# Kernel optimization log

Measured on AMD Instinct MI355X. Metric: run time of the kernel, lower is better.

Reference implementation:

```python
import jax, jax.numpy as jnp
import numpy as np

ROPE_THETA = 10000.0


def _rope(t, offset):
    """lucidrains-style interleaved RoPE. t: [b, s, h, d]."""
    s, d = t.shape[1], t.shape[-1]
    inv_freq = 1.0 / (ROPE_THETA ** (jnp.arange(0, d, 2, dtype=jnp.float32) / d))
    pos = jnp.arange(s, dtype=jnp.float32) + offset
    freqs = pos[:, None] * inv_freq[None, :]            # [s, d/2]
    freqs = jnp.repeat(freqs, 2, axis=-1)               # [s, d] interleaved
    cos = jnp.cos(freqs)[None, :, None, :].astype(t.dtype)
    sin = jnp.sin(freqs)[None, :, None, :].astype(t.dtype)
    x1 = t[..., 0::2]
    x2 = t[..., 1::2]
    rot = jnp.stack((-x2, x1), axis=-1).reshape(t.shape)  # rotate_half, interleaved
    return t * cos + rot * sin


def setup_inputs() -> dict:
    key = jax.random.key(0)
    ks = jax.random.split(key, 7)
    B, T, P, D, H, Hd = 4, 1024, 1024, 2048, 16, 128
    sc = 0.02
    return {
        "x": jax.random.normal(ks[0], (B, T, D), jnp.float32),
        "past_k": jax.random.normal(ks[1], (B, P, H, Hd), jnp.float32),
        "past_v": jax.random.normal(ks[2], (B, P, H, Hd), jnp.float32),
        "Wq": jax.random.normal(ks[3], (D, D), jnp.float32) * sc,
        "Wk": jax.random.normal(ks[4], (D, D), jnp.float32) * sc,
        "Wv": jax.random.normal(ks[5], (D, D), jnp.float32) * sc,
        "Wo": jax.random.normal(ks[6], (D, D), jnp.float32) * sc,
    }


def reference(x, past_k, past_v, Wq, Wk, Wv, Wo):
    B, T, D = x.shape
    H = past_k.shape[2]
    Hd = D // H
    P = past_k.shape[1]

    # QKV projections (bias-free) + head split: 'b t (h f) -> b t h f'
    q = (x @ Wq).reshape(B, T, H, Hd)
    k_new = (x @ Wk).reshape(B, T, H, Hd)
    v_new = (x @ Wv).reshape(B, T, H, Hd)

    # KV-cache concat along seq dim (-3)
    k = jnp.concatenate((past_k, k_new), axis=1)  # [B, P+T, H, Hd]
    v = jnp.concatenate((past_v, v_new), axis=1)

    # RoPE: K over full past+new from position 0; Q with offset = past length
    k = _rope(k, 0)
    q = _rope(q, P)

    # Flash-attn causal semantics (bottom-right aligned): q_i sees kv_j, j <= i + P
    scale = 1.0 / np.sqrt(Hd)
    scores = jnp.einsum("bthd,bshd->bhts", q, k) * scale  # [B, H, T, P+T]
    iq = jnp.arange(T)[:, None]
    jk = jnp.arange(P + T)[None, :]
    mask = jk <= (iq + P)
    scores = jnp.where(mask[None, None], scores, jnp.finfo(scores.dtype).min)
    attn = jax.nn.softmax(scores, axis=-1)
    y = jnp.einsum("bhts,bshd->bthd", attn, v)            # [B, T, H, Hd]

    y = y.reshape(B, T, D) @ Wo                            # output proj
    return y
```

## Files before the change

kernel.cpp:

```cpp
#include <hip/hip_runtime.h>

typedef unsigned short u16;
typedef float f32x4 __attribute__((ext_vector_type(4)));
typedef short bf16x8 __attribute__((ext_vector_type(8)));

#define GLOAD16(gp, lp) __builtin_amdgcn_global_load_lds( \
    (const __attribute__((address_space(1))) void*)(gp),  \
    (__attribute__((address_space(3))) void*)(lp), 16, 0, 0)

__device__ __forceinline__ float bf2f(u16 u) {
  union { unsigned int i; float f; } v; v.i = ((unsigned int)u) << 16; return v.f;
}
__device__ __forceinline__ u16 f2bf(float f) {
  unsigned int u = __float_as_uint(f);
  u += 0x7FFFu + ((u >> 16) & 1u);
  return (u16)(u >> 16);
}

__global__ void trig_kernel(float2* __restrict__ trig) {
  int idx = blockIdx.x * 256 + threadIdx.x;
  int pos = idx >> 6, i = idx & 63;
  double invf = pow(10000.0, -(double)i / 64.0);
  float ang = (float)pos * (float)invf;
  trig[idx] = make_float2(cosf(ang), sinf(ang));
}

__global__ void convert_x(const float* __restrict__ src, u16* __restrict__ dst) {
  size_t idx = (size_t)blockIdx.x * 256 + threadIdx.x;
  float4 v = *(const float4*)&src[idx * 4];
  *(ushort4*)&dst[idx * 4] = make_ushort4(f2bf(v.x), f2bf(v.y), f2bf(v.z), f2bf(v.w));
}

__global__ void transpose_w(const float* __restrict__ src, u16* __restrict__ dst) {
  __shared__ u16 tile[128][129];
  int k0 = blockIdx.x * 128, n0 = blockIdx.y * 128;
  int t = threadIdx.x;
  for (int j = 0; j < 16; ++j) {
    int flat = j * 1024 + t * 4;
    int r = flat >> 7, cl = flat & 127;
    float4 v = *(const float4*)&src[(size_t)(k0 + r) * 2048 + n0 + cl];
    tile[r][cl] = f2bf(v.x); tile[r][cl+1] = f2bf(v.y);
    tile[r][cl+2] = f2bf(v.z); tile[r][cl+3] = f2bf(v.w);
  }
  __syncthreads();
  for (int j = 0; j < 16; ++j) {
    int flat = j * 1024 + t * 4;
    int r = flat >> 7, cl = flat & 127;
    ushort4 o = make_ushort4(tile[cl][r], tile[cl+1][r], tile[cl+2][r], tile[cl+3][r]);
    *(ushort4*)&dst[(size_t)(n0 + r) * 2048 + k0 + cl] = o;
  }
}

template<int WF32>
__global__ void __launch_bounds__(256) gemm_bt(
    const u16* __restrict__ A, const u16* __restrict__ Bt,
    void* __restrict__ Cp, int ldc, int nbx, int kt_iters, int lda, int ldb)
{
  __shared__ __align__(16) u16 lds_a[4096];
  __shared__ __align__(16) u16 lds_b[4096];
  int nb = gridDim.x;
  int per = nb >> 3;
  int bid = blockIdx.x;
  int sw = (bid & 7) * per + (bid >> 3);
  int bm = sw / nbx, bn = sw % nbx;
  int tid = threadIdx.x, w = tid >> 6, lane = tid & 63;
  int wy = w >> 1, wx = w & 1, g = lane >> 4, c16 = lane & 15;

  const u16* ga0 = A  + (size_t)(bm * 128 + (2*w+0) * 16 + c16) * lda + g * 8;
  const u16* ga1 = A  + (size_t)(bm * 128 + (2*w+1) * 16 + c16) * lda + g * 8;
  const u16* gb0 = Bt + (size_t)(bn * 128 + (2*w+0) * 16 + c16) * ldb + g * 8;
  const u16* gb1 = Bt + (size_t)(bn * 128 + (2*w+1) * 16 + c16) * ldb + g * 8;
  u16* la0 = &lds_a[(2*w+0) * 512]; u16* la1 = &lds_a[(2*w+1) * 512];
  u16* lb0 = &lds_b[(2*w+0) * 512]; u16* lb1 = &lds_b[(2*w+1) * 512];

  f32x4 acc[4][4];
  const f32x4 vzero = {0.f, 0.f, 0.f, 0.f};
  #pragma unroll
  for (int i = 0; i < 4; ++i)
    #pragma unroll
    for (int j = 0; j < 4; ++j) acc[i][j] = vzero;

  for (int kt = 0; kt < kt_iters; ++kt) {
    int ko = kt * 32;
    __syncthreads();
    GLOAD16(ga0 + ko, la0); GLOAD16(ga1 + ko, la1);
    GLOAD16(gb0 + ko, lb0); GLOAD16(gb1 + ko, lb1);
    __syncthreads();
    bf16x8 af[4], bfv[4];
    #pragma unroll
    for (int f = 0; f < 4; ++f) af[f]  = *(const bf16x8*)&lds_a[(wy*4 + f) * 512 + lane * 8];
    #pragma unroll
    for (int f = 0; f < 4; ++f) bfv[f] = *(const bf16x8*)&lds_b[(wx*4 + f) * 512 + lane * 8];
    #pragma unroll
    for (int i = 0; i < 4; ++i)
      #pragma unroll
      for (int j = 0; j < 4; ++j)
        acc[i][j] = __builtin_amdgcn_mfma_f32_16x16x32_bf16(af[i], bfv[j], acc[i][j], 0, 0, 0);
  }

  #pragma unroll
  for (int i = 0; i < 4; ++i)
    #pragma unroll
    for (int j = 0; j < 4; ++j)
      #pragma unroll
      for (int r = 0; r < 4; ++r) {
        size_t row = (size_t)bm * 128 + wy * 64 + i * 16 + 4 * g + r;
        size_t col = (size_t)bn * 128 + wx * 64 + j * 16 + c16;
        if (WF32) ((float*)Cp)[row * ldc + col] = acc[i][j][r];
        else      ((u16*)Cp)[row * ldc + col]   = f2bf(acc[i][j][r]);
      }
}

__global__ void rope_q(u16* __restrict__ C1, const float2* __restrict__ trig) {
  int idx = blockIdx.x * 256 + threadIdx.x;
  int row = idx >> 10;
  int pi = idx & 1023;
  int h = pi >> 6, i = pi & 63;
  int pos = 1024 + (row & 1023);
  float2 cs = trig[pos * 64 + i];
  u16* p = &C1[(size_t)row * 6144 + h * 128 + 2 * i];
  ushort2 xv = *(const ushort2*)p;
  float x0 = bf2f(xv.x), x1 = bf2f(xv.y);
  const float SC = 0.088388347648318447f * 1.4426950408889634f;
  float y0 = (x0 * cs.x - x1 * cs.y) * SC;
  float y1 = (x1 * cs.x + x0 * cs.y) * SC;
  *(ushort2*)p = make_ushort2(f2bf(y0), f2bf(y1));
}

__global__ void build_k(const float* __restrict__ past_k, const u16* __restrict__ C1,
                        const float2* __restrict__ trig, u16* __restrict__ Kb) {
  int idx = blockIdx.x * 256 + threadIdx.x;
  int i = idx & 63;
  int s = (idx >> 6) & 2047;
  int bh = idx >> 17;
  int b = bh >> 4, h = bh & 15;
  float x0, x1;
  if (s < 1024) {
    const float* p = &past_k[(size_t)((b * 1024 + s) * 16 + h) * 128 + 2 * i];
    float2 v = *(const float2*)p;
    x0 = v.x; x1 = v.y;
  } else {
    ushort2 v = *(const ushort2*)&C1[(size_t)(b * 1024 + s - 1024) * 6144 + 2048 + h * 128 + 2 * i];
    x0 = bf2f(v.x); x1 = bf2f(v.y);
  }
  float2 cs = trig[s * 64 + i];
  float y0 = x0 * cs.x - x1 * cs.y;
  float y1 = x1 * cs.x + x0 * cs.y;
  *(ushort2*)&Kb[((size_t)bh * 2048 + s) * 128 + 2 * i] = make_ushort2(f2bf(y0), f2bf(y1));
}

__global__ void build_vt(const float* __restrict__ past_v, const u16* __restrict__ C1,
                         u16* __restrict__ Vt) {
  __shared__ u16 tile[128][129];
  int bh = blockIdx.x, st = blockIdx.y;
  int b = bh >> 4, h = bh & 15;
  int s0 = st * 128;
  int t = threadIdx.x;
  for (int j = 0; j < 16; ++j) {
    int flat = j * 1024 + t * 4;
    int sl = flat >> 7, dl = flat & 127;
    u16 a, bq, cq, dq;
    if (st < 8) {
      float4 v = *(const float4*)&past_v[(size_t)((b * 1024 + s0 + sl) * 16 + h) * 128 + dl];
      a = f2bf(v.x); bq = f2bf(v.y); cq = f2bf(v.z); dq = f2bf(v.w);
    } else {
      ushort4 v = *(const ushort4*)&C1[(size_t)(b * 1024 + s0 + sl - 1024) * 6144 + 4096 + h * 128 + dl];
      a = v.x; bq = v.y; cq = v.z; dq = v.w;
    }
    tile[sl][dl] = a; tile[sl][dl+1] = bq; tile[sl][dl+2] = cq; tile[sl][dl+3] = dq;
  }
  __syncthreads();
  for (int j = 0; j < 16; ++j) {
    int flat = j * 1024 + t * 4;
    int dl = flat >> 7, sl = flat & 127;
    ushort4 o = make_ushort4(tile[sl][dl], tile[sl+1][dl], tile[sl+2][dl], tile[sl+3][dl]);
    *(ushort4*)&Vt[((size_t)bh * 128 + dl) * 2048 + s0 + sl] = o;
  }
}

__global__ void __launch_bounds__(256) attn_kernel(
    const u16* __restrict__ Q, const u16* __restrict__ Kb,
    const u16* __restrict__ Vt, u16* __restrict__ Y)
{
  __shared__ __align__(16) u16 ldsK[8192];
  __shared__ __align__(16) u16 ldsV[8192];
  __shared__ __align__(16) u16 ldsP[4][1024];
  int qt = blockIdx.x, bh = blockIdx.y;
  int b = bh >> 4, h = bh & 15;
  int w = threadIdx.x >> 6, lane = threadIdx.x & 63;
  int g = lane >> 4, c16 = lane & 15;

  bf16x8 qf[4];
  {
    const u16* qp = Q + (size_t)(b * 1024 + qt * 64 + w * 16 + c16) * 6144 + h * 128 + g * 8;
    #pragma unroll
    for (int c = 0; c < 4; ++c) qf[c] = *(const bf16x8*)(qp + c * 32);
  }
  const u16* Kh = Kb + (size_t)bh * 2048 * 128;
  const u16* Vh = Vt + (size_t)bh * 128 * 2048;
  const u16* gk[4]; const u16* gv[4];
  #pragma unroll
  for (int j = 0; j < 4; ++j) {
    int u = w * 4 + j;
    gk[j] = Kh + (size_t)(16 * w + c16) * 128 + j * 32 + g * 8;
    int dt = u >> 1, sc = u & 1;
    gv[j] = Vh + (size_t)(16 * dt + c16) * 2048 + sc * 32 + g * 8;
  }

  const f32x4 vzero = {0.f, 0.f, 0.f, 0.f};
  f32x4 yacc[8];
  #pragma unroll
  for (int dt = 0; dt < 8; ++dt) yacc[dt] = vzero;
  float m_run[4] = {-3e38f, -3e38f, -3e38f, -3e38f};
  float l_run[4] = {0.f, 0.f, 0.f, 0.f};

  int ntiles = 17 + qt;
  for (int it = 0; it < ntiles; ++it) {
    int s0 = it * 64;
    __syncthreads();
    #pragma unroll
    for (int j = 0; j < 4; ++j) GLOAD16(gk[j] + (size_t)s0 * 128, &ldsK[(w * 4 + j) * 512]);
    #pragma unroll
    for (int j = 0; j < 4; ++j) GLOAD16(gv[j] + s0, &ldsV[(w * 4 + j) * 512]);
    __syncthreads();

    f32x4 sc_[4];
    #pragma unroll
    for (int t = 0; t < 4; ++t) sc_[t] = vzero;
    #pragma unroll
    for (int t = 0; t < 4; ++t)
      #pragma unroll
      for (int c = 0; c < 4; ++c) {
        bf16x8 kbf = *(const bf16x8*)&ldsK[(t * 4 + c) * 512 + lane * 8];
        sc_[t] = __builtin_amdgcn_mfma_f32_16x16x32_bf16(qf[c], kbf, sc_[t], 0, 0, 0);
      }
    if (it == ntiles - 1) {
      #pragma unroll
      for (int t = 0; t < 4; ++t)
        #pragma unroll
        for (int r = 0; r < 4; ++r)
          if (16 * t + c16 > 16 * w + 4 * g + r) sc_[t][r] = -3e38f;
    }

    float tmax[4];
    #pragma unroll
    for (int r = 0; r < 4; ++r)
      tmax[r] = fmaxf(fmaxf(sc_[0][r], sc_[1][r]), fmaxf(sc_[2][r], sc_[3][r]));
    #pragma unroll
    for (int off = 1; off < 16; off <<= 1)
      #pragma unroll
      for (int r = 0; r < 4; ++r) tmax[r] = fmaxf(tmax[r], __shfl_xor(tmax[r], off));

    float m_new[4], alpha[4];
    #pragma unroll
    for (int r = 0; r < 4; ++r) {
      m_new[r] = fmaxf(m_run[r], tmax[r]);
      alpha[r] = exp2f(m_run[r] - m_new[r]);
      m_run[r] = m_new[r];
    }
    float psum[4] = {0.f, 0.f, 0.f, 0.f};
    #pragma unroll
    for (int t = 0; t < 4; ++t)
      #pragma unroll
      for (int r = 0; r < 4; ++r) {
        float p = exp2f(sc_[t][r] - m_new[r]);
        psum[r] += p;
        int row = 4 * g + r, key = 16 * t + c16;
        ldsP[w][row * 64 + (((key >> 3) ^ (row & 7)) << 3) + (key & 7)] = f2bf(p);
      }
    #pragma unroll
    for (int off = 1; off < 16; off <<= 1)
      #pragma unroll
      for (int r = 0; r < 4; ++r) psum[r] += __shfl_xor(psum[r], off);
    #pragma unroll
    for (int r = 0; r < 4; ++r) l_run[r] = l_run[r] * alpha[r] + psum[r];
    #pragma unroll
    for (int dt = 0; dt < 8; ++dt)
      #pragma unroll
      for (int r = 0; r < 4; ++r) yacc[dt][r] *= alpha[r];

    bf16x8 pa[2];
    #pragma unroll
    for (int s2 = 0; s2 < 2; ++s2)
      pa[s2] = *(const bf16x8*)&ldsP[w][c16 * 64 + (((g + 4 * s2) ^ (c16 & 7)) << 3)];

    #pragma unroll
    for (int dt = 0; dt < 8; ++dt)
      #pragma unroll
      for (int s2 = 0; s2 < 2; ++s2) {
        bf16x8 vb = *(const bf16x8*)&ldsV[(dt * 2 + s2) * 512 + lane * 8];
        yacc[dt] = __builtin_amdgcn_mfma_f32_16x16x32_bf16(pa[s2], vb, yacc[dt], 0, 0, 0);
      }
  }

  float linv[4];
  #pragma unroll
  for (int r = 0; r < 4; ++r) linv[r] = 1.0f / l_run[r];
  size_t ybase = (size_t)(b * 1024 + qt * 64 + w * 16) * 2048 + h * 128;
  #pragma unroll
  for (int dt = 0; dt < 8; ++dt)
    #pragma unroll
    for (int r = 0; r < 4; ++r)
      Y[ybase + (size_t)(4 * g + r) * 2048 + dt * 16 + c16] = f2bf(yacc[dt][r] * linv[r]);
}

extern "C" void kernel_launch(void* const* d_in, const int* in_sizes, int n_in,
                              void* d_out, int out_size, void* d_ws, size_t ws_size,
                              hipStream_t stream) {
  const float* x  = (const float*)d_in[0];
  const float* pk = (const float*)d_in[1];
  const float* pv = (const float*)d_in[2];
  const float* Wq = (const float*)d_in[3];
  const float* Wk = (const float*)d_in[4];
  const float* Wv = (const float*)d_in[5];
  const float* Wo = (const float*)d_in[6];
  float* out = (float*)d_out;
  char* ws = (char*)d_ws;
  size_t off = 0;
  float2* trig = (float2*)(ws + off); off += (size_t)2048 * 64 * 8;
  u16* xbf     = (u16*)(ws + off);    off += (size_t)4096 * 2048 * 2;
  u16* wqkvt   = (u16*)(ws + off);    off += (size_t)6144 * 2048 * 2;
  u16* wot     = (u16*)(ws + off);    off += (size_t)2048 * 2048 * 2;
  u16* c1      = (u16*)(ws + off);    off += (size_t)4096 * 6144 * 2;
  u16* kb      = (u16*)(ws + off);    off += (size_t)64 * 2048 * 128 * 2;
  u16* vt      = (u16*)(ws + off);    off += (size_t)64 * 128 * 2048 * 2;
  u16* yb      = (u16*)(ws + off);    off += (size_t)4096 * 2048 * 2;

  trig_kernel<<<512, 256, 0, stream>>>(trig);
  convert_x<<<8192, 256, 0, stream>>>(x, xbf);
  transpose_w<<<dim3(16, 16), 256, 0, stream>>>(Wq, wqkvt);
  transpose_w<<<dim3(16, 16), 256, 0, stream>>>(Wk, wqkvt + (size_t)2048 * 2048);
  transpose_w<<<dim3(16, 16), 256, 0, stream>>>(Wv, wqkvt + (size_t)2 * 2048 * 2048);
  transpose_w<<<dim3(16, 16), 256, 0, stream>>>(Wo, wot);
  gemm_bt<0><<<1536, 256, 0, stream>>>(xbf, wqkvt, (void*)c1, 6144, 48, 64, 2048, 2048);
  rope_q<<<16384, 256, 0, stream>>>(c1, trig);
  build_k<<<32768, 256, 0, stream>>>(pk, c1, trig, kb);
  build_vt<<<dim3(64, 16), 256, 0, stream>>>(pv, c1, vt);
  attn_kernel<<<dim3(16, 64), 256, 0, stream>>>(c1, kb, vt, yb);
  gemm_bt<1><<<512, 256, 0, stream>>>(yb, wot, (void*)out, 2048, 16, 64, 2048, 2048);
}
```

Baseline: 681.9 us.

## Double-buffer K/V tiles in attention and schedule heavy causal tiles first

The attention kernel now uses two LDS buffers for the K and V tiles. The next tile's global-to-LDS load is issued before computing on the current one, which removes one barrier per iteration and overlaps memory latency with MFMA work. The launch grid is flattened and remapped so that blocks with the longest causal loops (highest query tiles) start first, with an XCD-aware interleave of the (batch, head) work. The cost is double the K/V LDS footprint, which may reduce how many blocks fit on each CU.

```diff
diff --git a/kernel.cpp b/kernel.cpp
--- a/kernel.cpp
+++ b/kernel.cpp
@@ -182,10 +182,13 @@
     const u16* __restrict__ Q, const u16* __restrict__ Kb,
     const u16* __restrict__ Vt, u16* __restrict__ Y)
 {
-  __shared__ __align__(16) u16 ldsK[8192];
-  __shared__ __align__(16) u16 ldsV[8192];
+  __shared__ __align__(16) u16 ldsK[2][8192];
+  __shared__ __align__(16) u16 ldsV[2][8192];
   __shared__ __align__(16) u16 ldsP[4][1024];
-  int qt = blockIdx.x, bh = blockIdx.y;
+  int bid = blockIdx.x;
+  int work = (bid & 7) * 128 + (bid >> 3);
+  int bh = work >> 4;
+  int qt = 15 - (work & 15);
   int b = bh >> 4, h = bh & 15;
   int w = threadIdx.x >> 6, lane = threadIdx.x & 63;
   int g = lane >> 4, c16 = lane & 15;
@@ -215,14 +218,24 @@
   float l_run[4] = {0.f, 0.f, 0.f, 0.f};
 
   int ntiles = 17 + qt;
+
+  #pragma unroll
+  for (int j = 0; j < 4; ++j) GLOAD16(gk[j], &ldsK[0][(w * 4 + j) * 512]);
+  #pragma unroll
+  for (int j = 0; j < 4; ++j) GLOAD16(gv[j], &ldsV[0][(w * 4 + j) * 512]);
+
   for (int it = 0; it < ntiles; ++it) {
-    int s0 = it * 64;
+    int cur = it & 1;
     __syncthreads();
-    #pragma unroll
-    for (int j = 0; j < 4; ++j) GLOAD16(gk[j] + (size_t)s0 * 128, &ldsK[(w * 4 + j) * 512]);
-    #pragma unroll
-    for (int j = 0; j < 4; ++j) GLOAD16(gv[j] + s0, &ldsV[(w * 4 + j) * 512]);
-    __syncthreads();
+    if (it + 1 < ntiles) {
+      int s1 = (it + 1) * 64;
+      #pragma unroll
+      for (int j = 0; j < 4; ++j) GLOAD16(gk[j] + (size_t)s1 * 128, &ldsK[cur ^ 1][(w * 4 + j) * 512]);
+      #pragma unroll
+      for (int j = 0; j < 4; ++j) GLOAD16(gv[j] + s1, &ldsV[cur ^ 1][(w * 4 + j) * 512]);
+    }
+    const u16* kb_l = &ldsK[cur][0];
+    const u16* vb_l = &ldsV[cur][0];
 
     f32x4 sc_[4];
     #pragma unroll
@@ -231,7 +244,7 @@
     for (int t = 0; t < 4; ++t)
       #pragma unroll
       for (int c = 0; c < 4; ++c) {
-        bf16x8 kbf = *(const bf16x8*)&ldsK[(t * 4 + c) * 512 + lane * 8];
+        bf16x8 kbf = *(const bf16x8*)&kb_l[(t * 4 + c) * 512 + lane * 8];
         sc_[t] = __builtin_amdgcn_mfma_f32_16x16x32_bf16(qf[c], kbf, sc_[t], 0, 0, 0);
       }
     if (it == ntiles - 1) {
@@ -288,7 +301,7 @@
     for (int dt = 0; dt < 8; ++dt)
       #pragma unroll
       for (int s2 = 0; s2 < 2; ++s2) {
-        bf16x8 vb = *(const bf16x8*)&ldsV[(dt * 2 + s2) * 512 + lane * 8];
+        bf16x8 vb = *(const bf16x8*)&vb_l[(dt * 2 + s2) * 512 + lane * 8];
         yacc[dt] = __builtin_amdgcn_mfma_f32_16x16x32_bf16(pa[s2], vb, yacc[dt], 0, 0, 0);
       }
   }
@@ -336,6 +349,6 @@
   rope_q<<<16384, 256, 0, stream>>>(c1, trig);
   build_k<<<32768, 256, 0, stream>>>(pk, c1, trig, kb);
   build_vt<<<dim3(64, 16), 256, 0, stream>>>(pv, c1, vt);
-  attn_kernel<<<dim3(16, 64), 256, 0, stream>>>(c1, kb, vt, yb);
+  attn_kernel<<<1024, 256, 0, stream>>>(c1, kb, vt, yb);
   gemm_bt<1><<<512, 256, 0, stream>>>(yb, wot, (void*)out, 2048, 16, 64, 2048, 2048);
 }
```

Result: no change. 669.4 us (-1.8%).
